# Optimization experiments

Measured on AMD Instinct MI355X. Metric: run time of the kernel, lower is better.

The kernel has to match this reference:

```python
import jax, jax.numpy as jnp
import numpy as np

MIN_C = 1e-5   # base_c * DYNAMIC_CURVATURE_MIN_RATIO
MAX_C = 10.0   # base_c * DYNAMIC_CURVATURE_MAX_RATIO
T = 0.7
EPS = 1e-7
B, IN_DIM, HID, OUT_DIM = 4096, 4096, 4096, 1024


def _artanh(x):
    x = jnp.clip(x, -1.0 + 1e-5, 1.0 - 1e-5)
    return 0.5 * jnp.log1p(2.0 * x / (1.0 - x))


def _mobius_scalar_mul(r, x, c):
    # r: python float, x: [B,D], c: [B,1] per-row curvature
    sqrt_c = jnp.sqrt(c)
    norm = jnp.clip(jnp.linalg.norm(x, axis=-1, keepdims=True), EPS)
    arg = jnp.clip(sqrt_c * norm, EPS, 1.0 - 1e-5)
    return jnp.tanh(r * _artanh(arg)) * x / (sqrt_c * norm)


def _mobius_add(x, y, c):
    xy = jnp.sum(x * y, axis=-1, keepdims=True)
    x2 = jnp.sum(x * x, axis=-1, keepdims=True)
    y2 = jnp.sum(y * y, axis=-1, keepdims=True)
    num = (1.0 + 2.0 * c * xy + c * y2) * x + (1.0 - c * x2) * y
    den = 1.0 + 2.0 * c * xy + c * c * x2 * y2
    return num / jnp.clip(den, EPS)


def poincare_ball_layer(h, u, c, t):
    # geodesic-style layer: ((1-t) (*) h) (+) (t (*) u) on the Poincare ball
    return _mobius_add(_mobius_scalar_mul(1.0 - t, h, c),
                       _mobius_scalar_mul(t, u, c), c)


def setup_inputs() -> dict:
    key = jax.random.key(0)
    ks = jax.random.split(key, 8)
    std = 0.02  # WEIGHT_INIT_STD_IMPROVED
    return {
        "x": jax.random.normal(ks[0], (B, IN_DIM), jnp.float32),
        "W1": jax.random.normal(ks[1], (IN_DIM, HID), jnp.float32) * std,
        "b1": jnp.zeros((HID,), jnp.float32),
        "W2": jax.random.normal(ks[2], (HID, HID), jnp.float32) * std,
        "b2": jnp.zeros((HID,), jnp.float32),
        "Wout": jax.random.normal(ks[3], (HID, OUT_DIM), jnp.float32) * std,
        "bout": jnp.zeros((OUT_DIM,), jnp.float32),
        "curv_feat": jax.random.normal(ks[4], (16,), jnp.float32) * 0.01,
        "curv_scale": jnp.ones((1,), jnp.float32) * 0.1,
        "proj": jax.random.normal(ks[5], (IN_DIM, 16), jnp.float32),
    }


def reference(x, W1, b1, W2, b2, Wout, bout, curv_feat, curv_scale, proj):
    x_flat = x.reshape(x.shape[0], -1)
    h = jnp.tanh(x_flat @ W1 + b1)            # [B, HID]
    u = jax.nn.sigmoid(h @ W2 + b2)           # [B, HID]
    # adaptive curvature prediction (vectorized over batch)
    x_red = x_flat @ proj                     # [B, 16]
    feat_inter = x_red @ curv_feat            # [B]
    adj = jax.nn.sigmoid(feat_inter + curv_scale[0])
    c = MIN_C + (MAX_C - MIN_C) * adj         # [B]
    c = jnp.clip(c, MIN_C, MAX_C)[:, None]    # [B, 1]
    z = poincare_ball_layer(h, u, c, T)
    # NaN fallback per row (mirrors torch per-sample isnan check)
    z = jnp.where(jnp.any(jnp.isnan(z), axis=1, keepdims=True), h, z)
    return z @ Wout + bout
```

## Files before the change

kernel.cpp:

```cpp
#include <hip/hip_runtime.h>
#include <hip/hip_bf16.h>
#include <math.h>


typedef __attribute__((ext_vector_type(8))) __bf16 bf16x8;
typedef __attribute__((ext_vector_type(4))) float  f32x4;
typedef __attribute__((ext_vector_type(8))) unsigned short us8;

constexpr int BATCH = 4096;
constexpr int IND   = 4096;
constexpr int HIDD  = 4096;
constexpr int OUTD  = 1024;
constexpr float T_C  = 0.7f;
constexpr float MINC = 1e-5f;
constexpr float MAXC = 10.0f;
constexpr float EPSV = 1e-7f;

__device__ __forceinline__ float bf2f(unsigned int us) {
    return __uint_as_float(us << 16);
}
__device__ __forceinline__ unsigned short f2bf(float f) {
    unsigned int u = __float_as_uint(f);
    u = (u + 0x7FFFu + ((u >> 16) & 1u)) >> 16;
    return (unsigned short)u;
}
__device__ __forceinline__ void stage16(const char* src, unsigned short* dst) {
    __builtin_amdgcn_global_load_lds(
        (const __attribute__((address_space(1))) unsigned int*)src,
        (__attribute__((address_space(3))) unsigned int*)dst, 16, 0, 0);
}

__global__ __launch_bounds__(256)
void cast_curv(const float* __restrict__ x, const float* __restrict__ v,
               const float* __restrict__ cs,
               unsigned short* __restrict__ xb, float* __restrict__ c)
{
    const int row = blockIdx.x;
    const float* xr = x + (size_t)row * IND;
    unsigned short* ob = xb + (size_t)row * IND;
    float s = 0.f;
    for (int i = threadIdx.x; i < IND / 4; i += 256) {
        float4 w  = ((const float4*)xr)[i];
        float4 vv = ((const float4*)v)[i];
        s += w.x * vv.x + w.y * vv.y + w.z * vv.z + w.w * vv.w;
        ushort4 o;
        o.x = f2bf(w.x); o.y = f2bf(w.y); o.z = f2bf(w.z); o.w = f2bf(w.w);
        ((ushort4*)ob)[i] = o;
    }
    #pragma unroll
    for (int o = 32; o > 0; o >>= 1) s += __shfl_down(s, o, 64);
    __shared__ float red[4];
    if ((threadIdx.x & 63) == 0) red[threadIdx.x >> 6] = s;
    __syncthreads();
    if (threadIdx.x == 0) {
        float tot = red[0] + red[1] + red[2] + red[3];
        float adj = 1.0f / (1.0f + expf(-(tot + cs[0])));
        float cc  = MINC + (MAXC - MINC) * adj;
        c[row] = fminf(fmaxf(cc, MINC), MAXC);
    }
}

__global__ __launch_bounds__(256)
void transpose_cast64(const float* __restrict__ in, unsigned short* __restrict__ out,
                      int K, int N)
{
    __shared__ float tile[64][65];
    const int k0 = blockIdx.y * 64;
    const int n0 = blockIdx.x * 64;
    const int t = threadIdx.x;
    #pragma unroll
    for (int i = 0; i < 4; i++) {
        const int idx = i * 256 + t;
        const int r = idx >> 4, c4 = (idx & 15) * 4;
        float4 v = *(const float4*)(&in[(size_t)(k0 + r) * N + n0 + c4]);
        tile[r][c4 + 0] = v.x; tile[r][c4 + 1] = v.y;
        tile[r][c4 + 2] = v.z; tile[r][c4 + 3] = v.w;
    }
    __syncthreads();
    #pragma unroll
    for (int j = 0; j < 2; j++) {
        const int idx = j * 256 + t;
        const int r = idx >> 3, c8 = (idx & 7) * 8;
        us8 o;
        #pragma unroll
        for (int e = 0; e < 8; e++) o[e] = f2bf(tile[c8 + e][r]);
        *(us8*)(&out[(size_t)(n0 + r) * K + k0 + c8]) = o;
    }
}

template<int EPI>
__global__ __launch_bounds__(512, 2)
void gemm256(const unsigned short* __restrict__ A,
             const unsigned short* __restrict__ Bt,
             const float* __restrict__ bias,
             unsigned short* __restrict__ outp,
             int N, int K)
{
    __shared__ unsigned short lds[4 * 256 * 64];

    const int t = threadIdx.x;
    const int w = t >> 6, l = t & 63;
    const int wr = w >> 2, wc = w & 3;
    const int lr = l & 15, lg = l >> 4;

    const int nwg = gridDim.x * gridDim.y;
    const int bid = blockIdx.y * gridDim.x + blockIdx.x;
    const int q8 = nwg >> 3, r8 = nwg & 7;
    const int xcd = bid & 7, off = bid >> 3;
    const int wgid = (xcd < r8 ? xcd * (q8 + 1) : r8 * (q8 + 1) + (xcd - r8) * q8) + off;
    const int by = wgid / gridDim.x;
    const int bx = wgid % gridDim.x;

    const int row0 = by * 256, col0 = bx * 256;
    const unsigned short* Ab = A  + (size_t)row0 * K;
    const unsigned short* Bb = Bt + (size_t)col0 * K;
    const int NT = K >> 6;

    f32x4 acc[8][4] = {};

    const int id0 = t, id1 = 512 + t;
    const int r0 = id0 >> 3, r1 = id1 >> 3;
    const int cb0 = (id0 & 7) * 16, cb1 = (id1 & 7) * 16;
    const int s0 = cb0 ^ ((r0 & 7) << 4), s1 = cb1 ^ ((r1 & 7) << 4);
    const size_t K2 = (size_t)K * 2;
    const char* pA00 = (const char*)Ab + (size_t)r0 * K2 + s0;
    const char* pA01 = (const char*)Ab + (size_t)r1 * K2 + s1;
    const char* pA10 = pA00 + 128 * K2;
    const char* pA11 = pA01 + 128 * K2;
    const char* pB00 = (const char*)Bb + (size_t)r0 * K2 + s0;
    const char* pB01 = (const char*)Bb + (size_t)r1 * K2 + s1;
    const char* pB10 = pB00 + 128 * K2;
    const char* pB11 = pB01 + 128 * K2;
    const int dA0a = id0 * 8,          dA0b = id1 * 8;
    const int dA1a = 8192 + id0 * 8,   dA1b = 8192 + id1 * 8;
    const int dB0a = 32768 + id0 * 8,  dB0b = 32768 + id1 * 8;
    const int dB1a = 40960 + id0 * 8,  dB1b = 40960 + id1 * 8;

    const int sw = (lr & 7) << 4;
    const int c0 = (lg * 16) ^ sw;
    const int c1 = (64 + lg * 16) ^ sw;
    const int aofc0 = (wr * 16 + lr) * 128 + c0;
    const int aofc1 = (wr * 16 + lr) * 128 + c1;
    const int bofc0 = 65536 + (wc * 64 + lr) * 128 + c0;
    const int bofc1 = 65536 + (wc * 64 + lr) * 128 + c1;
    const char* ldsb = (const char*)lds;

    stage16(pA00, lds + dA0a); stage16(pA01, lds + dA0b);
    stage16(pB00, lds + dB0a); stage16(pB01, lds + dB0b);
    stage16(pB10, lds + dB1a); stage16(pB11, lds + dB1b);
    stage16(pA10, lds + dA1a); stage16(pA11, lds + dA1b);
    asm volatile("s_waitcnt vmcnt(2)" ::: "memory");
    __builtin_amdgcn_s_barrier();

    for (int kt = 0; kt < NT; ++kt) {
        const int buf = kt & 1, nb = buf ^ 1;
        const bool pre = (kt + 1 < NT);
        pA00 += 128; pA01 += 128; pA10 += 128; pA11 += 128;
        pB00 += 128; pB01 += 128; pB10 += 128; pB11 += 128;
        const int bufby = buf * 32768;
        const int bsh   = nb * 16384;
        const char* rA0 = ldsb + bufby + aofc0;
        const char* rA1 = ldsb + bufby + aofc1;
        const char* rB0 = ldsb + bufby + bofc0;
        const char* rB1 = ldsb + bufby + bofc1;

        bf16x8 bfk[4], afk[4];

        #pragma unroll
        for (int ni = 0; ni < 4; ni++) bfk[ni] = *(const bf16x8*)(rB0 + ni * 2048);
        #pragma unroll
        for (int mi = 0; mi < 4; mi++) afk[mi] = *(const bf16x8*)(rA0 + mi * 4096);
        if (pre) {
            stage16(pA00, lds + bsh + dA0a); stage16(pA01, lds + bsh + dA0b);
            stage16(pB00, lds + bsh + dB0a); stage16(pB01, lds + bsh + dB0b);
        }
        __builtin_amdgcn_s_setprio(1);
        #pragma unroll
        for (int mi = 0; mi < 4; mi++)
            #pragma unroll
            for (int ni = 0; ni < 4; ni++)
                acc[mi][ni] = __builtin_amdgcn_mfma_f32_16x16x32_bf16(
                    afk[mi], bfk[ni], acc[mi][ni], 0, 0, 0);
        __builtin_amdgcn_s_setprio(0);
        if (pre) asm volatile("s_waitcnt vmcnt(4)" ::: "memory");
        else     asm volatile("s_waitcnt vmcnt(0)" ::: "memory");
        __builtin_amdgcn_s_barrier();

        #pragma unroll
        for (int mi = 0; mi < 4; mi++) afk[mi] = *(const bf16x8*)(rA0 + 16384 + mi * 4096);
        if (pre) {
            stage16(pB10, lds + bsh + dB1a); stage16(pB11, lds + bsh + dB1b);
            stage16(pA10, lds + bsh + dA1a); stage16(pA11, lds + bsh + dA1b);
        }
        __builtin_amdgcn_s_setprio(1);
        #pragma unroll
        for (int mi = 0; mi < 4; mi++)
            #pragma unroll
            for (int ni = 0; ni < 4; ni++)
                acc[4 + mi][ni] = __builtin_amdgcn_mfma_f32_16x16x32_bf16(
                    afk[mi], bfk[ni], acc[4 + mi][ni], 0, 0, 0);
        __builtin_amdgcn_s_setprio(0);
        __builtin_amdgcn_s_barrier();

        #pragma unroll
        for (int ni = 0; ni < 4; ni++) bfk[ni] = *(const bf16x8*)(rB1 + ni * 2048);
        #pragma unroll
        for (int mi = 0; mi < 4; mi++) afk[mi] = *(const bf16x8*)(rA1 + mi * 4096);
        __builtin_amdgcn_s_setprio(1);
        #pragma unroll
        for (int mi = 0; mi < 4; mi++)
            #pragma unroll
            for (int ni = 0; ni < 4; ni++)
                acc[mi][ni] = __builtin_amdgcn_mfma_f32_16x16x32_bf16(
                    afk[mi], bfk[ni], acc[mi][ni], 0, 0, 0);
        __builtin_amdgcn_s_setprio(0);
        __builtin_amdgcn_s_barrier();

        #pragma unroll
        for (int mi = 0; mi < 4; mi++) afk[mi] = *(const bf16x8*)(rA1 + 16384 + mi * 4096);
        __builtin_amdgcn_s_setprio(1);
        #pragma unroll
        for (int mi = 0; mi < 4; mi++)
            #pragma unroll
            for (int ni = 0; ni < 4; ni++)
                acc[4 + mi][ni] = __builtin_amdgcn_mfma_f32_16x16x32_bf16(
                    afk[mi], bfk[ni], acc[4 + mi][ni], 0, 0, 0);
        __builtin_amdgcn_s_setprio(0);
        if (pre) asm volatile("s_waitcnt vmcnt(2)" ::: "memory");
        else     asm volatile("s_waitcnt vmcnt(0)" ::: "memory");
        __builtin_amdgcn_s_barrier();
    }

    const int colb = col0 + wc * 64;
    #pragma unroll
    for (int ni = 0; ni < 4; ni++) {
        const int cg = colb + ni * 16 + lr;
        const float bv = bias[cg];
        #pragma unroll
        for (int mi = 0; mi < 8; mi++) {
            #pragma unroll
            for (int r = 0; r < 4; r++) {
                const int rg = row0 + wr * 16 + mi * 32 + lg * 4 + r;
                float v = acc[mi][ni][r] + bv;
                if constexpr (EPI == 0) v = tanhf(v);
                else                    v = 1.0f / (1.0f + expf(-v));
                outp[(size_t)rg * N + cg] = f2bf(v);
            }
        }
    }
}

__global__ __launch_bounds__(512, 2)
void gemm_out128(const unsigned short* __restrict__ A,
                 const unsigned short* __restrict__ Bt,
                 const float* __restrict__ bias,
                 float* __restrict__ outp,
                 int N, int K)
{
    __shared__ unsigned short lds[32768];

    const int t = threadIdx.x;
    const int w = t >> 6, l = t & 63;
    const int wr = w >> 2, wc = w & 3;
    const int lr = l & 15, lg = l >> 4;

    const int nwg = gridDim.x * gridDim.y;
    const int bid = blockIdx.y * gridDim.x + blockIdx.x;
    const int q8 = nwg >> 3, r8 = nwg & 7;
    const int xcd = bid & 7, off = bid >> 3;
    const int wgid = (xcd < r8 ? xcd * (q8 + 1) : r8 * (q8 + 1) + (xcd - r8) * q8) + off;
    const int by = wgid / gridDim.x;
    const int bx = wgid % gridDim.x;

    const int row0 = by * 128, col0 = bx * 128;
    const unsigned short* Ab = A  + (size_t)row0 * K;
    const unsigned short* Bb = Bt + (size_t)col0 * K;
    const int NT = K >> 6;

    f32x4 acc[4][2] = {};

    const int sr = t >> 2;
    const int scb = ((t & 3) * 16) ^ ((sr & 3) << 4);
    const size_t K2 = (size_t)K * 2;
    const char* pAk0 = (const char*)Ab + (size_t)sr * K2 + scb;
    const char* pAk1 = pAk0 + 64;
    const char* pBk0 = (const char*)Bb + (size_t)sr * K2 + scb;
    const char* pBk1 = pBk0 + 64;
    const int dAk0 = t * 8,          dAk1 = 4096 + t * 8;
    const int dBk0 = 16384 + t * 8,  dBk1 = 20480 + t * 8;

    const int csw = (lg * 16) ^ ((lr & 3) << 4);
    const int aof = (wr * 64 + lr) * 64 + csw;
    const int bof = 32768 + (wc * 32 + lr) * 64 + csw;
    const char* ldsb = (const char*)lds;

    stage16(pAk0, lds + dAk0); stage16(pBk0, lds + dBk0);
    stage16(pAk1, lds + dAk1); stage16(pBk1, lds + dBk1);
    asm volatile("s_waitcnt vmcnt(2)" ::: "memory");
    __builtin_amdgcn_s_barrier();

    for (int kt = 0; kt < NT; ++kt) {
        const int buf = kt & 1, nb = buf ^ 1;
        const bool pre = (kt + 1 < NT);
        pAk0 += 128; pAk1 += 128; pBk0 += 128; pBk1 += 128;
        const int bufby = buf * 16384;
        const int bsh   = nb * 8192;
        const char* rA0 = ldsb + bufby + aof;
        const char* rB0 = ldsb + bufby + bof;
        const char* rA1 = rA0 + 8192;
        const char* rB1 = rB0 + 8192;

        bf16x8 af[4], bfr[2];

        #pragma unroll
        for (int nj = 0; nj < 2; nj++) bfr[nj] = *(const bf16x8*)(rB0 + nj * 1024);
        #pragma unroll
        for (int mi = 0; mi < 4; mi++) af[mi] = *(const bf16x8*)(rA0 + mi * 1024);
        if (pre) { stage16(pAk0, lds + bsh + dAk0); stage16(pBk0, lds + bsh + dBk0); }
        __builtin_amdgcn_s_setprio(1);
        #pragma unroll
        for (int mi = 0; mi < 4; mi++)
            #pragma unroll
            for (int nj = 0; nj < 2; nj++)
                acc[mi][nj] = __builtin_amdgcn_mfma_f32_16x16x32_bf16(
                    af[mi], bfr[nj], acc[mi][nj], 0, 0, 0);
        __builtin_amdgcn_s_setprio(0);
        if (pre) asm volatile("s_waitcnt vmcnt(2)" ::: "memory");
        else     asm volatile("s_waitcnt vmcnt(0)" ::: "memory");
        __builtin_amdgcn_s_barrier();

        #pragma unroll
        for (int nj = 0; nj < 2; nj++) bfr[nj] = *(const bf16x8*)(rB1 + nj * 1024);
        #pragma unroll
        for (int mi = 0; mi < 4; mi++) af[mi] = *(const bf16x8*)(rA1 + mi * 1024);
        if (pre) { stage16(pAk1, lds + bsh + dAk1); stage16(pBk1, lds + bsh + dBk1); }
        __builtin_amdgcn_s_setprio(1);
        #pragma unroll
        for (int mi = 0; mi < 4; mi++)
            #pragma unroll
            for (int nj = 0; nj < 2; nj++)
                acc[mi][nj] = __builtin_amdgcn_mfma_f32_16x16x32_bf16(
                    af[mi], bfr[nj], acc[mi][nj], 0, 0, 0);
        __builtin_amdgcn_s_setprio(0);
        if (pre) asm volatile("s_waitcnt vmcnt(2)" ::: "memory");
        else     asm volatile("s_waitcnt vmcnt(0)" ::: "memory");
        __builtin_amdgcn_s_barrier();
    }

    #pragma unroll
    for (int nj = 0; nj < 2; nj++) {
        const int cg = col0 + wc * 32 + nj * 16 + lr;
        const float bv = bias[cg];
        #pragma unroll
        for (int mi = 0; mi < 4; mi++)
            #pragma unroll
            for (int r = 0; r < 4; r++) {
                const int rg = row0 + wr * 64 + mi * 16 + lg * 4 + r;
                outp[(size_t)rg * N + cg] = acc[mi][nj][r] + bv;
            }
    }
}

__global__ __launch_bounds__(256)
void proj_cf(const float* __restrict__ proj, const float* __restrict__ cf,
             float* __restrict__ v)
{
    int i = blockIdx.x * 256 + threadIdx.x;
    if (i < IND) {
        float s = 0.f;
        #pragma unroll
        for (int j = 0; j < 16; j++) s += proj[i * 16 + j] * cf[j];
        v[i] = s;
    }
}

__global__ __launch_bounds__(256)
void poincare_kernel(const unsigned short* __restrict__ hb,
                     const unsigned short* __restrict__ ub,
                     const float* __restrict__ c,
                     unsigned short* __restrict__ zb)
{
    const int row = blockIdx.x;
    const int t = threadIdx.x;
    const size_t base = (size_t)row * HIDD;

    float hv[16], uv[16];
    float h2 = 0.f, u2 = 0.f, hu = 0.f;
    #pragma unroll
    for (int q = 0; q < 2; q++) {
        const int e0 = (q * 256 + t) * 8;
        uint4 hc = *(const uint4*)(hb + base + e0);
        uint4 uc = *(const uint4*)(ub + base + e0);
        const unsigned int hw[4] = {hc.x, hc.y, hc.z, hc.w};
        const unsigned int uw[4] = {uc.x, uc.y, uc.z, uc.w};
        #pragma unroll
        for (int i = 0; i < 4; i++) {
            float h0 = bf2f(hw[i] & 0xFFFFu), h1 = bf2f(hw[i] >> 16);
            float u0 = bf2f(uw[i] & 0xFFFFu), u1 = bf2f(uw[i] >> 16);
            hv[q * 8 + 2 * i]     = h0; hv[q * 8 + 2 * i + 1] = h1;
            uv[q * 8 + 2 * i]     = u0; uv[q * 8 + 2 * i + 1] = u1;
            h2 += h0 * h0 + h1 * h1;
            u2 += u0 * u0 + u1 * u1;
            hu += h0 * u0 + h1 * u1;
        }
    }
    #pragma unroll
    for (int o = 32; o > 0; o >>= 1) {
        h2 += __shfl_down(h2, o, 64);
        u2 += __shfl_down(u2, o, 64);
        hu += __shfl_down(hu, o, 64);
    }
    __shared__ float red[3][4];
    const int w = t >> 6;
    if ((t & 63) == 0) { red[0][w] = h2; red[1][w] = u2; red[2][w] = hu; }
    __syncthreads();
    h2 = red[0][0] + red[0][1] + red[0][2] + red[0][3];
    u2 = red[1][0] + red[1][1] + red[1][2] + red[1][3];
    hu = red[2][0] + red[2][1] + red[2][2] + red[2][3];

    const float cc = c[row];
    const float sc = sqrtf(cc);
    float nh = fmaxf(sqrtf(h2), EPSV);
    float nu = fmaxf(sqrtf(u2), EPSV);
    float ah = fminf(fmaxf(sc * nh, EPSV), 1.0f - 1e-5f);
    float au = fminf(fmaxf(sc * nu, EPSV), 1.0f - 1e-5f);
    float ath = 0.5f * log1pf(2.0f * ah / (1.0f - ah));
    float atu = 0.5f * log1pf(2.0f * au / (1.0f - au));
    float alpha = tanhf((1.0f - T_C) * ath) / (sc * nh);
    float beta  = tanhf(T_C * atu) / (sc * nu);
    float x2 = alpha * alpha * h2;
    float y2 = beta * beta * u2;
    float xy = alpha * beta * hu;
    float den = 1.0f + 2.0f * cc * xy + cc * cc * x2 * y2;
    den = fmaxf(den, EPSV);
    float ca = (1.0f + 2.0f * cc * xy + cc * y2) * alpha / den;
    float cb = (1.0f - cc * x2) * beta / den;
    if (isnan(ca) || isnan(cb)) { ca = 1.0f; cb = 0.0f; }

    #pragma unroll
    for (int q = 0; q < 2; q++) {
        const int e0 = (q * 256 + t) * 8;
        unsigned int ow[4];
        #pragma unroll
        for (int i = 0; i < 4; i++) {
            float z0 = ca * hv[q * 8 + 2 * i]     + cb * uv[q * 8 + 2 * i];
            float z1 = ca * hv[q * 8 + 2 * i + 1] + cb * uv[q * 8 + 2 * i + 1];
            ow[i] = (unsigned int)f2bf(z0) | ((unsigned int)f2bf(z1) << 16);
        }
        *(uint4*)(zb + base + e0) = make_uint4(ow[0], ow[1], ow[2], ow[3]);
    }
}

extern "C" void kernel_launch(void* const* d_in, const int* in_sizes, int n_in,
                              void* d_out, int out_size, void* d_ws, size_t ws_size,
                              hipStream_t stream)
{
    const float* x    = (const float*)d_in[0];
    const float* W1   = (const float*)d_in[1];
    const float* b1   = (const float*)d_in[2];
    const float* W2   = (const float*)d_in[3];
    const float* b2   = (const float*)d_in[4];
    const float* Wout = (const float*)d_in[5];
    const float* bout = (const float*)d_in[6];
    const float* cf   = (const float*)d_in[7];
    const float* cs   = (const float*)d_in[8];
    const float* proj = (const float*)d_in[9];
    float* out = (float*)d_out;

    char* ws = (char*)d_ws;
    unsigned short* x_bf = (unsigned short*)(ws);
    unsigned short* w_bf = (unsigned short*)(ws + (33554432));
    unsigned short* h_bf = (unsigned short*)(ws + (67108864));
    unsigned short* u_bf = (unsigned short*)(ws + (100663296));
    float* vvec = (float*)(ws + 134217728);
    float* cvec = (float*)(ws + 134217728 + 16384);

    proj_cf<<<IND / 256, 256, 0, stream>>>(proj, cf, vvec);
    cast_curv<<<BATCH, 256, 0, stream>>>(x, vvec, cs, x_bf, cvec);

    transpose_cast64<<<dim3(HIDD / 64, IND / 64), 256, 0, stream>>>(W1, w_bf, IND, HIDD);
    gemm256<0><<<dim3(HIDD / 256, BATCH / 256), 512, 0, stream>>>(x_bf, w_bf, b1, h_bf, HIDD, IND);

    transpose_cast64<<<dim3(HIDD / 64, HIDD / 64), 256, 0, stream>>>(W2, w_bf, HIDD, HIDD);
    gemm256<1><<<dim3(HIDD / 256, BATCH / 256), 512, 0, stream>>>(h_bf, w_bf, b2, u_bf, HIDD, HIDD);

    poincare_kernel<<<BATCH, 256, 0, stream>>>(h_bf, u_bf, cvec, x_bf);

    transpose_cast64<<<dim3(OUTD / 64, HIDD / 64), 256, 0, stream>>>(Wout, w_bf, HIDD, OUTD);
    gemm_out128<<<dim3(OUTD / 128, BATCH / 128), 512, 0, stream>>>(x_bf, w_bf, bout, out, OUTD, HIDD);
}
```

Before: 386.1 us.

## Switch 256x256 GEMM to 32x32x16 MFMA with per-wave fragment-ordered LDS layout

Rewrites the main 256x256 GEMM mainloop to use 32x32x16 bf16 MFMA instructions instead of 16x16x32, with each wave staging its own 32-row strips of A and B into LDS in the exact lane order the MFMA fragments are read. This replaces the swizzled layout with direct per-lane 16-byte reads, and splits each K tile into four sub-steps, each with a barrier and a finer-grained vmcnt wait. The larger MFMA shape halves the number of MFMA issues and LDS fragment loads per FLOP. In exchange there are more barriers per K tile and a new epilogue row mapping. The stage16 signature change also forces byte-offset fixes in the smaller GEMM.

```diff
diff --git a/kernel.cpp b/kernel.cpp
--- a/kernel.cpp
+++ b/kernel.cpp
@@ -3,9 +3,10 @@
 #include <math.h>
 
 
-typedef __attribute__((ext_vector_type(8))) __bf16 bf16x8;
-typedef __attribute__((ext_vector_type(4))) float  f32x4;
-typedef __attribute__((ext_vector_type(8))) unsigned short us8;
+typedef __attribute__((ext_vector_type(8)))  __bf16 bf16x8;
+typedef __attribute__((ext_vector_type(4)))  float  f32x4;
+typedef __attribute__((ext_vector_type(16))) float  f32x16;
+typedef __attribute__((ext_vector_type(8)))  unsigned short us8;
 
 constexpr int BATCH = 4096;
 constexpr int IND   = 4096;
@@ -24,7 +25,7 @@
     u = (u + 0x7FFFu + ((u >> 16) & 1u)) >> 16;
     return (unsigned short)u;
 }
-__device__ __forceinline__ void stage16(const char* src, unsigned short* dst) {
+__device__ __forceinline__ void stage16(const char* src, const char* dst) {
     __builtin_amdgcn_global_load_lds(
         (const __attribute__((address_space(1))) unsigned int*)src,
         (__attribute__((address_space(3))) unsigned int*)dst, 16, 0, 0);
@@ -96,12 +97,12 @@
              unsigned short* __restrict__ outp,
              int N, int K)
 {
-    __shared__ unsigned short lds[4 * 256 * 64];
+    __shared__ unsigned short lds[65536];
 
     const int t = threadIdx.x;
     const int w = t >> 6, l = t & 63;
     const int wr = w >> 2, wc = w & 3;
-    const int lr = l & 15, lg = l >> 4;
+    const int lq = l & 31, lh = l >> 5;
 
     const int nwg = gridDim.x * gridDim.y;
     const int bid = blockIdx.y * gridDim.x + blockIdx.x;
@@ -116,131 +117,77 @@
     const unsigned short* Bb = Bt + (size_t)col0 * K;
     const int NT = K >> 6;
 
-    f32x4 acc[8][4] = {};
-
-    const int id0 = t, id1 = 512 + t;
-    const int r0 = id0 >> 3, r1 = id1 >> 3;
-    const int cb0 = (id0 & 7) * 16, cb1 = (id1 & 7) * 16;
-    const int s0 = cb0 ^ ((r0 & 7) << 4), s1 = cb1 ^ ((r1 & 7) << 4);
+    f32x16 acc[4][2] = {};
+
     const size_t K2 = (size_t)K * 2;
-    const char* pA00 = (const char*)Ab + (size_t)r0 * K2 + s0;
-    const char* pA01 = (const char*)Ab + (size_t)r1 * K2 + s1;
-    const char* pA10 = pA00 + 128 * K2;
-    const char* pA11 = pA01 + 128 * K2;
-    const char* pB00 = (const char*)Bb + (size_t)r0 * K2 + s0;
-    const char* pB01 = (const char*)Bb + (size_t)r1 * K2 + s1;
-    const char* pB10 = pB00 + 128 * K2;
-    const char* pB11 = pB01 + 128 * K2;
-    const int dA0a = id0 * 8,          dA0b = id1 * 8;
-    const int dA1a = 8192 + id0 * 8,   dA1b = 8192 + id1 * 8;
-    const int dB0a = 32768 + id0 * 8,  dB0b = 32768 + id1 * 8;
-    const int dB1a = 40960 + id0 * 8,  dB1b = 40960 + id1 * 8;
-
-    const int sw = (lr & 7) << 4;
-    const int c0 = (lg * 16) ^ sw;
-    const int c1 = (64 + lg * 16) ^ sw;
-    const int aofc0 = (wr * 16 + lr) * 128 + c0;
-    const int aofc1 = (wr * 16 + lr) * 128 + c1;
-    const int bofc0 = 65536 + (wc * 64 + lr) * 128 + c0;
-    const int bofc1 = 65536 + (wc * 64 + lr) * 128 + c1;
+    const char* pA = (const char*)Ab + (size_t)(w * 32 + lq) * K2 + lh * 16;
+    const char* pB = (const char*)Bb + (size_t)(w * 32 + lq) * K2 + lh * 16;
+    char* dA = (char*)lds + w * 4096 + l * 16;
+    char* dB = (char*)lds + 65536 + w * 4096 + l * 16;
+
+    const int rAbase = (wr * 4) * 4096 + l * 16;
+    const int rBbase = 65536 + (wc * 2) * 4096 + l * 16;
     const char* ldsb = (const char*)lds;
 
-    stage16(pA00, lds + dA0a); stage16(pA01, lds + dA0b);
-    stage16(pB00, lds + dB0a); stage16(pB01, lds + dB0b);
-    stage16(pB10, lds + dB1a); stage16(pB11, lds + dB1b);
-    stage16(pA10, lds + dA1a); stage16(pA11, lds + dA1b);
-    asm volatile("s_waitcnt vmcnt(2)" ::: "memory");
+    #pragma unroll
+    for (int p = 0; p < 4; p++) {
+        stage16(pA + p * 32, dA + p * 1024);
+        stage16(pB + p * 32, dB + p * 1024);
+    }
+    asm volatile("s_waitcnt vmcnt(0)" ::: "memory");
     __builtin_amdgcn_s_barrier();
 
     for (int kt = 0; kt < NT; ++kt) {
         const int buf = kt & 1, nb = buf ^ 1;
         const bool pre = (kt + 1 < NT);
-        pA00 += 128; pA01 += 128; pA10 += 128; pA11 += 128;
-        pB00 += 128; pB01 += 128; pB10 += 128; pB11 += 128;
-        const int bufby = buf * 32768;
-        const int bsh   = nb * 16384;
-        const char* rA0 = ldsb + bufby + aofc0;
-        const char* rA1 = ldsb + bufby + aofc1;
-        const char* rB0 = ldsb + bufby + bofc0;
-        const char* rB1 = ldsb + bufby + bofc1;
-
-        bf16x8 bfk[4], afk[4];
-
-        #pragma unroll
-        for (int ni = 0; ni < 4; ni++) bfk[ni] = *(const bf16x8*)(rB0 + ni * 2048);
-        #pragma unroll
-        for (int mi = 0; mi < 4; mi++) afk[mi] = *(const bf16x8*)(rA0 + mi * 4096);
-        if (pre) {
-            stage16(pA00, lds + bsh + dA0a); stage16(pA01, lds + bsh + dA0b);
-            stage16(pB00, lds + bsh + dB0a); stage16(pB01, lds + bsh + dB0b);
+        pA += 128; pB += 128;
+        const char* rA = ldsb + buf * 32768 + rAbase;
+        const char* rB = ldsb + buf * 32768 + rBbase;
+        char* sA = dA + nb * 32768;
+        char* sB = dB + nb * 32768;
+
+        #pragma unroll
+        for (int p = 0; p < 4; p++) {
+            bf16x8 bfr[2], afr[4];
+            bfr[0] = *(const bf16x8*)(rB + p * 1024);
+            bfr[1] = *(const bf16x8*)(rB + 4096 + p * 1024);
+            #pragma unroll
+            for (int mi = 0; mi < 4; mi++)
+                afr[mi] = *(const bf16x8*)(rA + mi * 4096 + p * 1024);
+            if (pre) {
+                stage16(pA + p * 32, sA + p * 1024);
+                stage16(pB + p * 32, sB + p * 1024);
+            }
+            __builtin_amdgcn_s_setprio(1);
+            #pragma unroll
+            for (int mi = 0; mi < 4; mi++)
+                #pragma unroll
+                for (int ni = 0; ni < 2; ni++)
+                    acc[mi][ni] = __builtin_amdgcn_mfma_f32_32x32x16_bf16(
+                        afr[mi], bfr[ni], acc[mi][ni], 0, 0, 0);
+            __builtin_amdgcn_s_setprio(0);
+            if (pre) {
+                asm volatile("s_waitcnt vmcnt(6)" ::: "memory");
+            } else {
+                if (p == 0)      asm volatile("s_waitcnt vmcnt(4)" ::: "memory");
+                else if (p == 1) asm volatile("s_waitcnt vmcnt(2)" ::: "memory");
+                else if (p == 2) asm volatile("s_waitcnt vmcnt(0)" ::: "memory");
+            }
+            __builtin_amdgcn_s_barrier();
         }
-        __builtin_amdgcn_s_setprio(1);
-        #pragma unroll
-        for (int mi = 0; mi < 4; mi++)
-            #pragma unroll
-            for (int ni = 0; ni < 4; ni++)
-                acc[mi][ni] = __builtin_amdgcn_mfma_f32_16x16x32_bf16(
-                    afk[mi], bfk[ni], acc[mi][ni], 0, 0, 0);
-        __builtin_amdgcn_s_setprio(0);
-        if (pre) asm volatile("s_waitcnt vmcnt(4)" ::: "memory");
-        else     asm volatile("s_waitcnt vmcnt(0)" ::: "memory");
-        __builtin_amdgcn_s_barrier();
-
-        #pragma unroll
-        for (int mi = 0; mi < 4; mi++) afk[mi] = *(const bf16x8*)(rA0 + 16384 + mi * 4096);
-        if (pre) {
-            stage16(pB10, lds + bsh + dB1a); stage16(pB11, lds + bsh + dB1b);
-            stage16(pA10, lds + bsh + dA1a); stage16(pA11, lds + bsh + dA1b);
-        }
-        __builtin_amdgcn_s_setprio(1);
-        #pragma unroll
-        for (int mi = 0; mi < 4; mi++)
-            #pragma unroll
-            for (int ni = 0; ni < 4; ni++)
-                acc[4 + mi][ni] = __builtin_amdgcn_mfma_f32_16x16x32_bf16(
-                    afk[mi], bfk[ni], acc[4 + mi][ni], 0, 0, 0);
-        __builtin_amdgcn_s_setprio(0);
-        __builtin_amdgcn_s_barrier();
-
-        #pragma unroll
-        for (int ni = 0; ni < 4; ni++) bfk[ni] = *(const bf16x8*)(rB1 + ni * 2048);
-        #pragma unroll
-        for (int mi = 0; mi < 4; mi++) afk[mi] = *(const bf16x8*)(rA1 + mi * 4096);
-        __builtin_amdgcn_s_setprio(1);
-        #pragma unroll
-        for (int mi = 0; mi < 4; mi++)
-            #pragma unroll
-            for (int ni = 0; ni < 4; ni++)
-                acc[mi][ni] = __builtin_amdgcn_mfma_f32_16x16x32_bf16(
-                    afk[mi], bfk[ni], acc[mi][ni], 0, 0, 0);
-        __builtin_amdgcn_s_setprio(0);
-        __builtin_amdgcn_s_barrier();
-
-        #pragma unroll
-        for (int mi = 0; mi < 4; mi++) afk[mi] = *(const bf16x8*)(rA1 + 16384 + mi * 4096);
-        __builtin_amdgcn_s_setprio(1);
-        #pragma unroll
-        for (int mi = 0; mi < 4; mi++)
-            #pragma unroll
-            for (int ni = 0; ni < 4; ni++)
-                acc[4 + mi][ni] = __builtin_amdgcn_mfma_f32_16x16x32_bf16(
-                    afk[mi], bfk[ni], acc[4 + mi][ni], 0, 0, 0);
-        __builtin_amdgcn_s_setprio(0);
-        if (pre) asm volatile("s_waitcnt vmcnt(2)" ::: "memory");
-        else     asm volatile("s_waitcnt vmcnt(0)" ::: "memory");
-        __builtin_amdgcn_s_barrier();
     }
 
     const int colb = col0 + wc * 64;
-    #pragma unroll
-    for (int ni = 0; ni < 4; ni++) {
-        const int cg = colb + ni * 16 + lr;
+    const int rowb = row0 + wr * 128 + lh * 4;
+    #pragma unroll
+    for (int ni = 0; ni < 2; ni++) {
+        const int cg = colb + ni * 32 + lq;
         const float bv = bias[cg];
         #pragma unroll
-        for (int mi = 0; mi < 8; mi++) {
-            #pragma unroll
-            for (int r = 0; r < 4; r++) {
-                const int rg = row0 + wr * 16 + mi * 32 + lg * 4 + r;
+        for (int mi = 0; mi < 4; mi++) {
+            #pragma unroll
+            for (int r = 0; r < 16; r++) {
+                const int rg = rowb + mi * 32 + (r & 3) + 8 * (r >> 2);
                 float v = acc[mi][ni][r] + bv;
                 if constexpr (EPI == 0) v = tanhf(v);
                 else                    v = 1.0f / (1.0f + expf(-v));
@@ -286,16 +233,16 @@
     const char* pAk1 = pAk0 + 64;
     const char* pBk0 = (const char*)Bb + (size_t)sr * K2 + scb;
     const char* pBk1 = pBk0 + 64;
-    const int dAk0 = t * 8,          dAk1 = 4096 + t * 8;
-    const int dBk0 = 16384 + t * 8,  dBk1 = 20480 + t * 8;
+    const int dAk0 = t * 16,          dAk1 = 8192 + t * 16;
+    const int dBk0 = 32768 + t * 16,  dBk1 = 40960 + t * 16;
 
     const int csw = (lg * 16) ^ ((lr & 3) << 4);
     const int aof = (wr * 64 + lr) * 64 + csw;
     const int bof = 32768 + (wc * 32 + lr) * 64 + csw;
-    const char* ldsb = (const char*)lds;
-
-    stage16(pAk0, lds + dAk0); stage16(pBk0, lds + dBk0);
-    stage16(pAk1, lds + dAk1); stage16(pBk1, lds + dBk1);
+    char* ldsc = (char*)lds;
+
+    stage16(pAk0, ldsc + dAk0); stage16(pBk0, ldsc + dBk0);
+    stage16(pAk1, ldsc + dAk1); stage16(pBk1, ldsc + dBk1);
     asm volatile("s_waitcnt vmcnt(2)" ::: "memory");
     __builtin_amdgcn_s_barrier();
 
@@ -304,9 +251,9 @@
         const bool pre = (kt + 1 < NT);
         pAk0 += 128; pAk1 += 128; pBk0 += 128; pBk1 += 128;
         const int bufby = buf * 16384;
-        const int bsh   = nb * 8192;
-        const char* rA0 = ldsb + bufby + aof;
-        const char* rB0 = ldsb + bufby + bof;
+        const int bsh   = nb * 16384;
+        const char* rA0 = (const char*)lds + bufby + aof;
+        const char* rB0 = (const char*)lds + bufby + bof;
         const char* rA1 = rA0 + 8192;
         const char* rB1 = rB0 + 8192;
 
@@ -316,7 +263,7 @@
         for (int nj = 0; nj < 2; nj++) bfr[nj] = *(const bf16x8*)(rB0 + nj * 1024);
         #pragma unroll
         for (int mi = 0; mi < 4; mi++) af[mi] = *(const bf16x8*)(rA0 + mi * 1024);
-        if (pre) { stage16(pAk0, lds + bsh + dAk0); stage16(pBk0, lds + bsh + dBk0); }
+        if (pre) { stage16(pAk0, ldsc + bsh + dAk0); stage16(pBk0, ldsc + bsh + dBk0); }
         __builtin_amdgcn_s_setprio(1);
         #pragma unroll
         for (int mi = 0; mi < 4; mi++)
@@ -333,7 +280,7 @@
         for (int nj = 0; nj < 2; nj++) bfr[nj] = *(const bf16x8*)(rB1 + nj * 1024);
         #pragma unroll
         for (int mi = 0; mi < 4; mi++) af[mi] = *(const bf16x8*)(rA1 + mi * 1024);
-        if (pre) { stage16(pAk1, lds + bsh + dAk1); stage16(pBk1, lds + bsh + dBk1); }
+        if (pre) { stage16(pAk1, ldsc + bsh + dAk1); stage16(pBk1, ldsc + bsh + dBk1); }
         __builtin_amdgcn_s_setprio(1);
         #pragma unroll
         for (int mi = 0; mi < 4; mi++)
```

New measurement: 464.5 us. 20.3% more time.
